# Kernel tuning notes

Hardware: AMD Instinct MI355X
Metric: run time of the kernel (lower is better)

## Reference

```python
import jax, jax.numpy as jnp
import numpy as np

NUM_HEADS = 8


def setup_inputs() -> dict:
    key = jax.random.key(0)
    B, T, N, C = 16, 24, 716, 256
    H = NUM_HEADS
    D = C // H
    ks = jax.random.split(key, 14)

    def w(k, shape, scale=0.02):
        return jax.random.normal(k, shape, dtype=jnp.float32) * scale

    return {
        "x": jax.random.normal(ks[0], (B, T, N, C), dtype=jnp.float32),
        # nn.Linear weights stored PyTorch-style [out, in]
        "Wq": w(ks[1], (C, C)), "bq": w(ks[2], (C,)),
        "Wk": w(ks[3], (C, C)), "bk": w(ks[4], (C,)),
        "Wv": w(ks[5], (C, C)), "bv": w(ks[6], (C,)),
        "Wo": w(ks[7], (C, C)), "bo": w(ks[8], (C,)),
        # grouped conv1d (kernel_size=1) weights, squeezed: [out_ch, in_ch_per_group]
        "w1": w(ks[9], (C, D)), "b1": w(ks[10], (C,)),
        "w2": w(ks[11], (3 * C, D)), "b2": w(ks[12], (3 * C,)),
    }


def reference(x, Wq, bq, Wk, bk, Wv, bv, Wo, bo, w1, b1, w2, b2):
    B, T, N, C = x.shape
    H = NUM_HEADS
    D = C // H
    BT = B * T
    scale = D ** -0.5

    xf = x.reshape(BT, N, C)
    # q, k, v: [BT, H, N, D]
    q = (xf @ Wq.T + bq).reshape(BT, N, H, D).transpose(0, 2, 1, 3)
    k = (xf @ Wk.T + bk).reshape(BT, N, H, D).transpose(0, 2, 1, 3)
    v = (xf @ Wv.T + bv).reshape(BT, N, H, D).transpose(0, 2, 1, 3)

    # linear attention: kv outer-product [BT, H, D, D], scaled by (scale/N)
    kv = jnp.einsum('bhnd,bhne->bhde', k, v) * (scale / N)
    attn = jnp.einsum('bhnd,bhde->bhne', q, kv)
    # mean-pooled correction term
    kmean = k.mean(axis=2)  # [BT, H, D]
    vmean = v.mean(axis=2)  # [BT, H, D]
    qk = jnp.einsum('bhnd,bhd->bhn', q, kmean) * scale  # [BT, H, N]
    xa = attn + (1.0 - qk)[..., None] * vmean[:, :, None, :]
    xa = xa.transpose(0, 2, 1, 3).reshape(BT, N, C)

    # dynamic per-channel 3-tap kernel weights from node-mean features
    m = xf.mean(axis=1).reshape(BT, H, D)  # grouped input [BT, H, D]
    h1 = jnp.einsum('bgi,goi->bgo', m, w1.reshape(H, D, D)) + b1.reshape(H, D)
    h1 = jax.nn.gelu(h1, approximate=False)
    h2 = jnp.einsum('bgi,goi->bgo', h1, w2.reshape(H, 3 * D, D)) + b2.reshape(H, 3 * D)
    rw = h2.reshape(BT, C, 3)  # per-(sample, channel) 3-tap kernel

    # depthwise conv1d over node axis with groups = BT*C (cross-correlation)
    vc = v.transpose(0, 1, 3, 2).reshape(BT, C, N)
    vp = jnp.pad(vc, ((0, 0), (0, 0), (1, 1)))
    res = (rw[:, :, 0:1] * vp[:, :, 0:N]
           + rw[:, :, 1:2] * vp[:, :, 1:N + 1]
           + rw[:, :, 2:3] * vp[:, :, 2:N + 2])  # [BT, C, N]

    out = (xa + res.transpose(0, 2, 1)).reshape(B, T, N, C)
    return out @ Wo.T + bo
```

## Files before the change

### kernel.cpp

```cpp
#include <hip/hip_runtime.h>
#include <hip/hip_bf16.h>
#include <math.h>

typedef __attribute__((ext_vector_type(8))) short short8;
typedef __attribute__((ext_vector_type(4))) short sv4;
typedef __attribute__((ext_vector_type(4))) float f32x4;
typedef unsigned int u32;

#define BT_ 384
#define N_ 716
#define C_ 256
#define H_ 8
#define D_ 32
#define MROWS (BT_ * N_)
#define NT_ (MROWS / 64)
#define SCALE_ 0.17677669529663687f
#define INVN_ (1.0f / 716.0f)

__device__ __forceinline__ void gload_lds16(const void* g, void* l) {
    __builtin_amdgcn_global_load_lds(
        (const __attribute__((address_space(1))) u32*)g,
        (__attribute__((address_space(3))) u32*)l, 16, 0, 0);
}

__global__ void prep_weights(const float* __restrict__ Wq, const float* __restrict__ bq,
                             const float* __restrict__ Wk, const float* __restrict__ bk,
                             const float* __restrict__ Wv, const float* __restrict__ bv,
                             const float* __restrict__ Wo,
                             __hip_bfloat16* __restrict__ wqkv, float* __restrict__ bqkv,
                             __hip_bfloat16* __restrict__ wo) {
    int idx = blockIdx.x * 256 + threadIdx.x;
    if (idx < 768 * 256) {
        int o = idx >> 8, c = idx & 255;
        const float* W = (o < 256) ? Wq : ((o < 512) ? Wk : Wv);
        int oo = o & 255;
        wqkv[idx] = __float2bfloat16(W[oo * 256 + c]);
    }
    if (idx < 256 * 256) wo[idx] = __float2bfloat16(Wo[idx]);
    if (idx < 768) bqkv[idx] = (idx < 256) ? bq[idx] : ((idx < 512) ? bk[idx - 256] : bv[idx - 512]);
}

__global__ __launch_bounds__(256)
void convert_x(const float* __restrict__ x, __hip_bfloat16* __restrict__ xb,
               float* __restrict__ msum) {
    int bt = blockIdx.x, chunk = blockIdx.y;
    int t = threadIdx.x;
    int c4 = (t & 63) * 4;
    int r0 = t >> 6;
    size_t base = ((size_t)bt * N_ + (size_t)chunk * 179) * C_;
    float s0 = 0.f, s1 = 0.f, s2 = 0.f, s3 = 0.f;
    for (int r = r0; r < 179; r += 4) {
        float4 f = *(const float4*)&x[base + (size_t)r * C_ + c4];
        union { sv4 v; __hip_bfloat16 h[4]; } u;
        u.h[0] = __float2bfloat16(f.x);
        u.h[1] = __float2bfloat16(f.y);
        u.h[2] = __float2bfloat16(f.z);
        u.h[3] = __float2bfloat16(f.w);
        *(sv4*)&xb[base + (size_t)r * C_ + c4] = u.v;
        s0 += f.x; s1 += f.y; s2 += f.z; s3 += f.w;
    }
    atomicAdd(&msum[bt * C_ + c4 + 0], s0);
    atomicAdd(&msum[bt * C_ + c4 + 1], s1);
    atomicAdd(&msum[bt * C_ + c4 + 2], s2);
    atomicAdd(&msum[bt * C_ + c4 + 3], s3);
}

__global__ __launch_bounds__(256)
void mlp_rw(const float* __restrict__ msum, const float* __restrict__ w1,
            const float* __restrict__ b1, const float* __restrict__ w2,
            const float* __restrict__ b2, float* __restrict__ rw) {
    int bt = blockIdx.x;
    int t = threadIdx.x;
    __shared__ float m_l[256];
    __shared__ float h1_l[256];
    m_l[t] = msum[bt * 256 + t] * INVN_;
    __syncthreads();
    int g = t >> 5;
    float a = b1[t];
    #pragma unroll
    for (int i = 0; i < 32; ++i) a += m_l[g * 32 + i] * w1[t * 32 + i];
    h1_l[t] = 0.5f * a * (1.0f + erff(a * 0.70710678118654752f));
    __syncthreads();
    for (int o = t; o < 768; o += 256) {
        int gg = o / 96;
        float s = b2[o];
        #pragma unroll
        for (int i = 0; i < 32; ++i) s += h1_l[gg * 32 + i] * w2[o * 32 + i];
        rw[bt * 768 + o] = s;
    }
}

template<int NCOLS, int GRIDX, bool OUT_BF16>
__global__ __launch_bounds__(256, 2)
void gemm_persist(const __hip_bfloat16* __restrict__ A, const __hip_bfloat16* __restrict__ Bm,
                  const float* __restrict__ bias, void* __restrict__ outp) {
    __shared__ __align__(16) __hip_bfloat16 As[2][64 * 256];
    const int L = blockIdx.x;
    const int xcd = L & 7, w = L >> 3;
    const int cb = w % GRIDX;
    const int ib = xcd * 32 + w / GRIDX;
    const int tid = threadIdx.x;
    const int lane = tid & 63;
    const int wave = tid >> 6;
    const int wn = wave;
    const int colBase = cb * 128;
    const int l15 = lane & 15, lq = lane >> 4;
    const int lrow2 = lane >> 5;
    const int p = lane & 31;

    auto stageA = [&](int rt, int buf) {
        #pragma unroll
        for (int i = 0; i < 8; ++i) {
            int r = wave * 16 + 2 * i + lrow2;
            const __hip_bfloat16* g = A + ((size_t)rt * 64 + r) * 256 + ((p ^ (r & 7)) * 8);
            gload_lds16(g, &As[buf][(wave * 16 + 2 * i) * 256]);
        }
    };

    stageA(ib, 0);

    short8 bf[2][8];
    #pragma unroll
    for (int n = 0; n < 2; ++n)
        #pragma unroll
        for (int ks = 0; ks < 8; ++ks)
            bf[n][ks] = *(const short8*)&Bm[(size_t)(colBase + wn * 32 + n * 16 + l15) * 256 + ks * 32 + lq * 8];
    float biasr[2];
    #pragma unroll
    for (int n = 0; n < 2; ++n)
        biasr[n] = bias[colBase + wn * 32 + n * 16 + l15];

    asm volatile("s_waitcnt vmcnt(0)" ::: "memory");
    __builtin_amdgcn_s_barrier();

    int buf = 0;
    for (int rt = ib; rt < NT_; rt += 256) {
        int rtn = rt + 256;
        if (rtn < NT_) stageA(rtn, buf ^ 1);

        f32x4 acc[4][2] = {};
        #pragma unroll
        for (int ks = 0; ks < 8; ++ks) {
            short8 af[4];
            #pragma unroll
            for (int m = 0; m < 4; ++m) {
                int row = m * 16 + l15;
                af[m] = *(const short8*)&As[buf][row * 256 + (((ks * 4 + lq) ^ (row & 7)) * 8)];
            }
            #pragma unroll
            for (int m = 0; m < 4; ++m)
                #pragma unroll
                for (int n = 0; n < 2; ++n)
                    acc[m][n] = __builtin_amdgcn_mfma_f32_16x16x32_bf16(af[m], bf[n][ks], acc[m][n], 0, 0, 0);
        }
        asm volatile("s_waitcnt lgkmcnt(0)" ::: "memory");
        __builtin_amdgcn_s_barrier();

        if constexpr (OUT_BF16) {
            __hip_bfloat16* Cs = &As[buf][0];
            #pragma unroll
            for (int m = 0; m < 4; ++m)
                #pragma unroll
                for (int n = 0; n < 2; ++n) {
                    int col = wn * 32 + n * 16 + l15;
                    #pragma unroll
                    for (int j = 0; j < 4; ++j)
                        Cs[(m * 16 + lq * 4 + j) * 136 + col] =
                            __float2bfloat16(acc[m][n][j] + biasr[n]);
                }
            asm volatile("s_waitcnt lgkmcnt(0)" ::: "memory");
            __builtin_amdgcn_s_barrier();
            int row = tid >> 2, cq = tid & 3;
            __hip_bfloat16* og = (__hip_bfloat16*)outp + ((size_t)rt * 64 + row) * NCOLS + colBase;
            #pragma unroll
            for (int i = 0; i < 4; ++i) {
                int col = cq * 8 + i * 32;
                *(short8*)&og[col] = *(const short8*)&Cs[row * 136 + col];
            }
            asm volatile("s_waitcnt vmcnt(2) lgkmcnt(0)" ::: "memory");
            __builtin_amdgcn_s_barrier();
        } else {
            float* Cs = (float*)&As[buf][0];
            #pragma unroll
            for (int pp = 0; pp < 2; ++pp) {
                #pragma unroll
                for (int mm = 0; mm < 2; ++mm) {
                    int m = 2 * pp + mm;
                    #pragma unroll
                    for (int n = 0; n < 2; ++n) {
                        int col = wn * 32 + n * 16 + l15;
                        #pragma unroll
                        for (int j = 0; j < 4; ++j)
                            Cs[(mm * 16 + lq * 4 + j) * 132 + col] = acc[m][n][j] + biasr[n];
                    }
                }
                asm volatile("s_waitcnt lgkmcnt(0)" ::: "memory");
                __builtin_amdgcn_s_barrier();
                int row = tid >> 3, k = tid & 7;
                float* og = (float*)outp + ((size_t)rt * 64 + pp * 32 + row) * NCOLS + colBase;
                #pragma unroll
                for (int i = 0; i < 4; ++i) {
                    int col = k * 4 + i * 32;
                    *(float4*)&og[col] = *(const float4*)&Cs[row * 132 + col];
                }
                asm volatile("s_waitcnt lgkmcnt(0)" ::: "memory");
                __builtin_amdgcn_s_barrier();
            }
            asm volatile("s_waitcnt vmcnt(4) lgkmcnt(0)" ::: "memory");
            __builtin_amdgcn_s_barrier();
        }
        buf ^= 1;
    }
}

__global__ __launch_bounds__(512, 2)
void reduce_kv(const __hip_bfloat16* __restrict__ qkv, __hip_bfloat16* __restrict__ kv2t,
               float* __restrict__ vmeanb) {
    __shared__ __align__(16) __hip_bfloat16 T[512 * 64];
    const int bt = blockIdx.x;
    const int tid = threadIdx.x;
    const int lane = tid & 63;
    const int h = tid >> 6;
    const int l15 = lane & 15, lq = lane >> 4;
    const int co = tid >> 3;
    const int np3 = tid & 7;
    const size_t rowbase = (size_t)bt * N_;

    union S8 { short8 v; unsigned short u[8]; };
    const short8 zero8 = {0, 0, 0, 0, 0, 0, 0, 0};

    auto issue_loads = [&](int n0, S8* Aq, S8* Bq) {
        #pragma unroll
        for (int s = 0; s < 4; ++s) {
            int n = n0 + 2 * (np3 + 8 * s);
            Aq[s].v = (n < N_)     ? *(const short8*)&qkv[(rowbase + n) * 768 + 256 + co * 8] : zero8;
            Bq[s].v = (n + 1 < N_) ? *(const short8*)&qkv[(rowbase + n + 1) * 768 + 256 + co * 8] : zero8;
        }
    };
    auto write_lds = [&](S8* Aq, S8* Bq) {
        #pragma unroll
        for (int s = 0; s < 4; ++s) {
            int r = 2 * (np3 + 8 * s);
            int slotbase = ((r >> 3));
            #pragma unroll
            for (int j = 0; j < 8; ++j) {
                int c = co * 8 + j;
                u32 wv = (u32)Aq[s].u[j] | ((u32)Bq[s].u[j] << 16);
                int off = c * 64 + ((slotbase ^ (c & 7)) << 3) + (r & 7);
                *(u32*)&T[off] = wv;
            }
        }
    };

    S8 bufA[4], bufB[4], nxtA[4], nxtB[4];
    issue_loads(0, bufA, bufB);

    f32x4 acc[2][2] = {};
    f32x4 acck[2] = {};
    f32x4 accv[2] = {};
    S8 ones;
    #pragma unroll
    for (int j = 0; j < 8; ++j) ones.u[j] = 0x3F80;

    for (int chunk = 0; chunk < 12; ++chunk) {
        if (chunk < 11) issue_loads((chunk + 1) * 64, nxtA, nxtB);
        write_lds(bufA, bufB);
        __syncthreads();
        #pragma unroll
        for (int nc = 0; nc < 2; ++nc) {
            short8 af[2], bfr[2];
            int slot = nc * 4 + lq;
            #pragma unroll
            for (int dh = 0; dh < 2; ++dh) {
                int c = h * 32 + dh * 16 + l15;
                af[dh] = *(const short8*)&T[c * 64 + ((slot ^ (c & 7)) << 3)];
            }
            #pragma unroll
            for (int eh = 0; eh < 2; ++eh) {
                int c = 256 + h * 32 + eh * 16 + l15;
                bfr[eh] = *(const short8*)&T[c * 64 + ((slot ^ (c & 7)) << 3)];
            }
            #pragma unroll
            for (int dh = 0; dh < 2; ++dh)
                #pragma unroll
                for (int eh = 0; eh < 2; ++eh)
                    acc[dh][eh] = __builtin_amdgcn_mfma_f32_16x16x32_bf16(af[dh], bfr[eh], acc[dh][eh], 0, 0, 0);
            #pragma unroll
            for (int dh = 0; dh < 2; ++dh)
                acck[dh] = __builtin_amdgcn_mfma_f32_16x16x32_bf16(af[dh], ones.v, acck[dh], 0, 0, 0);
            #pragma unroll
            for (int eh = 0; eh < 2; ++eh)
                accv[eh] = __builtin_amdgcn_mfma_f32_16x16x32_bf16(ones.v, bfr[eh], accv[eh], 0, 0, 0);
        }
        __syncthreads();
        #pragma unroll
        for (int s = 0; s < 4; ++s) { bufA[s] = nxtA[s]; bufB[s] = nxtB[s]; }
    }

    const int bh = bt * 8 + h;
    #pragma unroll
    for (int eh = 0; eh < 2; ++eh) {
        int e = eh * 16 + l15;
        float vme = accv[eh][0] * INVN_;
        #pragma unroll
        for (int dh = 0; dh < 2; ++dh) {
            union { sv4 v; __hip_bfloat16 x[4]; } o;
            #pragma unroll
            for (int j = 0; j < 4; ++j) {
                float km = acck[dh][j] * INVN_;
                float val = acc[dh][eh][j] * (SCALE_ * INVN_) - SCALE_ * km * vme;
                o.x[j] = __float2bfloat16(val);
            }
            *(sv4*)&kv2t[(size_t)bh * 1024 + e * 32 + dh * 16 + lq * 4] = o.v;
        }
        if (lq == 0) vmeanb[bh * 32 + e] = vme;
    }
}

__global__ __launch_bounds__(256)
void fuse_z2(const __hip_bfloat16* __restrict__ qkv, const __hip_bfloat16* __restrict__ kv2t,
             const float* __restrict__ vmeanb, const float* __restrict__ rw,
             __hip_bfloat16* __restrict__ Z) {
    __shared__ __align__(16) __hip_bfloat16 attn[64][256];
    __shared__ __align__(16) __hip_bfloat16 kvl[8192];
    int bt = blockIdx.x;
    int n0 = blockIdx.y * 64;
    int rows = (N_ - n0 < 64) ? (N_ - n0) : 64;
    int t = threadIdx.x;
    const size_t rowbase = (size_t)bt * N_;

    {
        const __hip_bfloat16* src = kv2t + (size_t)bt * 8192;
        #pragma unroll
        for (int i = 0; i < 4; ++i) {
            int off = (t + i * 256) * 8;
            *(short8*)&kvl[off] = *(const short8*)&src[off];
        }
    }
    __syncthreads();

    {
        int lane = t & 63, wave = t >> 6;
        int l15 = lane & 15, lq = lane >> 4;
        int r0 = wave * 16;
        int gn = n0 + r0 + l15; if (gn > N_ - 1) gn = N_ - 1;
        const __hip_bfloat16* qrow = qkv + (rowbase + gn) * 768;
        #pragma unroll
        for (int h = 0; h < 8; ++h) {
            short8 af = *(const short8*)&qrow[h * 32 + lq * 8];
            #pragma unroll
            for (int half = 0; half < 2; ++half) {
                short8 bfr = *(const short8*)&kvl[h * 1024 + (half * 16 + l15) * 32 + lq * 8];
                f32x4 acc = {};
                acc = __builtin_amdgcn_mfma_f32_16x16x32_bf16(af, bfr, acc, 0, 0, 0);
                int col = h * 32 + half * 16 + l15;
                float vm = vmeanb[bt * 256 + col];
                #pragma unroll
                for (int j = 0; j < 4; ++j)
                    attn[r0 + lq * 4 + j][col] = __float2bfloat16(acc[j] + vm);
            }
        }
    }
    __syncthreads();

    {
        int tr = t >> 5;
        int c8 = (t & 31) * 8;
        float w0[8], w1_[8], w2_[8];
        #pragma unroll
        for (int u = 0; u < 8; ++u) {
            w0[u]  = rw[bt * 768 + (c8 + u) * 3 + 0];
            w1_[u] = rw[bt * 768 + (c8 + u) * 3 + 1];
            w2_[u] = rw[bt * 768 + (c8 + u) * 3 + 2];
        }
        int rbeg = tr * 8;
        if (rbeg < rows) {
            int rend = rbeg + 8; if (rend > rows) rend = rows;
            union U8 { short8 v; __hip_bfloat16 h[8]; };
            auto loadv = [&](int gn, float* dst) {
                if (gn >= 0 && gn < N_) {
                    U8 u; u.v = *(const short8*)&qkv[(rowbase + gn) * 768 + 512 + c8];
                    #pragma unroll
                    for (int uu = 0; uu < 8; ++uu) dst[uu] = __bfloat162float(u.h[uu]);
                } else {
                    #pragma unroll
                    for (int uu = 0; uu < 8; ++uu) dst[uu] = 0.0f;
                }
            };
            float vprev[8], vcur[8], vnext[8];
            loadv(n0 + rbeg - 1, vprev);
            loadv(n0 + rbeg, vcur);
            for (int r = rbeg; r < rend; ++r) {
                int gn = n0 + r;
                loadv(gn + 1, vnext);
                U8 at; at.v = *(const short8*)&attn[r][c8];
                U8 zv;
                #pragma unroll
                for (int u = 0; u < 8; ++u) {
                    float s = __bfloat162float(at.h[u]) + w0[u] * vprev[u]
                              + w1_[u] * vcur[u] + w2_[u] * vnext[u];
                    zv.h[u] = __float2bfloat16(s);
                }
                *(short8*)&Z[(rowbase + gn) * 256 + c8] = zv.v;
                #pragma unroll
                for (int u = 0; u < 8; ++u) { vprev[u] = vcur[u]; vcur[u] = vnext[u]; }
            }
        }
    }
}

extern "C" void kernel_launch(void* const* d_in, const int* in_sizes, int n_in,
                              void* d_out, int out_size, void* d_ws, size_t ws_size,
                              hipStream_t stream) {
    (void)in_sizes; (void)n_in; (void)out_size; (void)ws_size;
    const float* x  = (const float*)d_in[0];
    const float* Wq = (const float*)d_in[1];  const float* bq = (const float*)d_in[2];
    const float* Wk = (const float*)d_in[3];  const float* bk = (const float*)d_in[4];
    const float* Wv = (const float*)d_in[5];  const float* bv = (const float*)d_in[6];
    const float* Wo = (const float*)d_in[7];  const float* bo = (const float*)d_in[8];
    const float* w1 = (const float*)d_in[9];  const float* b1 = (const float*)d_in[10];
    const float* w2 = (const float*)d_in[11]; const float* b2 = (const float*)d_in[12];
    float* out = (float*)d_out;

    char* ws = (char*)d_ws;
    size_t off = 0;
    auto take = [&](size_t bytes) -> char* {
        char* p = ws + off;
        off = (off + bytes + 255) & ~(size_t)255;
        return p;
    };

    __hip_bfloat16* qkv   = (__hip_bfloat16*)take((size_t)MROWS * 768 * 2);
    __hip_bfloat16* xb    = (__hip_bfloat16*)take((size_t)MROWS * 256 * 2);
    __hip_bfloat16* Zbuf  = xb;
    __hip_bfloat16* wqkv  = (__hip_bfloat16*)take(768 * 256 * 2);
    __hip_bfloat16* wo    = (__hip_bfloat16*)take(256 * 256 * 2);
    float* bqkv   = (float*)take(768 * 4);
    float* msum   = (float*)take(384 * 256 * 4);
    float* rw     = (float*)take(384 * 768 * 4);
    __hip_bfloat16* kv2t = (__hip_bfloat16*)take((size_t)384 * 8192 * 2);
    float* vmeanb = (float*)take(384 * 256 * 4);

    hipMemsetAsync(msum, 0, 384 * 256 * 4, stream);

    prep_weights<<<768, 256, 0, stream>>>(Wq, bq, Wk, bk, Wv, bv, Wo, wqkv, bqkv, wo);
    convert_x<<<dim3(384, 4), 256, 0, stream>>>(x, xb, msum);
    mlp_rw<<<384, 256, 0, stream>>>(msum, w1, b1, w2, b2, rw);
    gemm_persist<768, 6, true><<<1536, 256, 0, stream>>>(xb, wqkv, bqkv, qkv);
    reduce_kv<<<384, 512, 0, stream>>>(qkv, kv2t, vmeanb);
    fuse_z2<<<dim3(384, 12), 256, 0, stream>>>(qkv, kv2t, vmeanb, rw, Zbuf);
    gemm_persist<256, 2, false><<<512, 256, 0, stream>>>(Zbuf, wo, bo, out);
}
```

Measured before the change: 542.5 us.

## Fuse output projection GEMM into attention/conv epilogue kernel

Merges the Z-building kernel with the final Wo projection. Each 512-thread block keeps its 64x256 Z tile in swizzled LDS, holds Wo fragments in registers, runs the MFMA GEMM in place and writes fp32 output through an LDS staging buffer. This removes the bf16 Z round trip to global memory and one kernel launch. In exchange, every block reloads the full Wo matrix into registers, register pressure rises, and the 716-row tail tiles waste some MFMA work.

```diff
diff --git a/kernel.cpp b/kernel.cpp
--- a/kernel.cpp
+++ b/kernel.cpp
@@ -317,93 +317,155 @@
     }
 }
 
-__global__ __launch_bounds__(256)
-void fuse_z2(const __hip_bfloat16* __restrict__ qkv, const __hip_bfloat16* __restrict__ kv2t,
-             const float* __restrict__ vmeanb, const float* __restrict__ rw,
-             __hip_bfloat16* __restrict__ Z) {
-    __shared__ __align__(16) __hip_bfloat16 attn[64][256];
-    __shared__ __align__(16) __hip_bfloat16 kvl[8192];
-    int bt = blockIdx.x;
-    int n0 = blockIdx.y * 64;
-    int rows = (N_ - n0 < 64) ? (N_ - n0) : 64;
-    int t = threadIdx.x;
+__global__ __launch_bounds__(512, 2)
+void fuse_zout(const __hip_bfloat16* __restrict__ qkv, const __hip_bfloat16* __restrict__ kv2t,
+               const float* __restrict__ vmeanb, const float* __restrict__ rw,
+               const __hip_bfloat16* __restrict__ wo, const float* __restrict__ bo,
+               float* __restrict__ outp) {
+    __shared__ __align__(16) __hip_bfloat16 AZ[64 * 256];
+    __shared__ __align__(16) char RB[17408];
+    __hip_bfloat16* kvl = (__hip_bfloat16*)RB;
+
+    const int bt = blockIdx.x;
+    const int n0 = blockIdx.y * 64;
+    const int rows = (N_ - n0 < 64) ? (N_ - n0) : 64;
+    const int t = threadIdx.x;
+    const int lane = t & 63;
+    const int w = t >> 6;
+    const int l15 = lane & 15, lq = lane >> 4;
     const size_t rowbase = (size_t)bt * N_;
+
+    short8 bf[2][8];
+    #pragma unroll
+    for (int n = 0; n < 2; ++n)
+        #pragma unroll
+        for (int ks = 0; ks < 8; ++ks)
+            bf[n][ks] = *(const short8*)&wo[(size_t)(w * 32 + n * 16 + l15) * 256 + ks * 32 + lq * 8];
+    float biasr[2];
+    #pragma unroll
+    for (int n = 0; n < 2; ++n) biasr[n] = bo[w * 32 + n * 16 + l15];
 
     {
         const __hip_bfloat16* src = kv2t + (size_t)bt * 8192;
         #pragma unroll
-        for (int i = 0; i < 4; ++i) {
-            int off = (t + i * 256) * 8;
+        for (int i = 0; i < 2; ++i) {
+            int off = (t + i * 512) * 8;
             *(short8*)&kvl[off] = *(const short8*)&src[off];
         }
     }
     __syncthreads();
 
     {
-        int lane = t & 63, wave = t >> 6;
-        int l15 = lane & 15, lq = lane >> 4;
-        int r0 = wave * 16;
+        int r0 = (w & 3) * 16;
+        int hb = (w >> 2) * 4;
         int gn = n0 + r0 + l15; if (gn > N_ - 1) gn = N_ - 1;
         const __hip_bfloat16* qrow = qkv + (rowbase + gn) * 768;
         #pragma unroll
-        for (int h = 0; h < 8; ++h) {
+        for (int hh = 0; hh < 4; ++hh) {
+            int h = hb + hh;
             short8 af = *(const short8*)&qrow[h * 32 + lq * 8];
             #pragma unroll
             for (int half = 0; half < 2; ++half) {
-                short8 bfr = *(const short8*)&kvl[h * 1024 + (half * 16 + l15) * 32 + lq * 8];
-                f32x4 acc = {};
-                acc = __builtin_amdgcn_mfma_f32_16x16x32_bf16(af, bfr, acc, 0, 0, 0);
+                short8 kb = *(const short8*)&kvl[h * 1024 + (half * 16 + l15) * 32 + lq * 8];
+                f32x4 a = {};
+                a = __builtin_amdgcn_mfma_f32_16x16x32_bf16(af, kb, a, 0, 0, 0);
                 int col = h * 32 + half * 16 + l15;
                 float vm = vmeanb[bt * 256 + col];
                 #pragma unroll
-                for (int j = 0; j < 4; ++j)
-                    attn[r0 + lq * 4 + j][col] = __float2bfloat16(acc[j] + vm);
+                for (int j = 0; j < 4; ++j) {
+                    int r = r0 + lq * 4 + j;
+                    AZ[r * 256 + ((((col >> 3) ^ (r & 7)) << 3) | (col & 7))] =
+                        __float2bfloat16(a[j] + vm);
+                }
             }
         }
     }
     __syncthreads();
 
     {
-        int tr = t >> 5;
-        int c8 = (t & 31) * 8;
-        float w0[8], w1_[8], w2_[8];
-        #pragma unroll
-        for (int u = 0; u < 8; ++u) {
-            w0[u]  = rw[bt * 768 + (c8 + u) * 3 + 0];
-            w1_[u] = rw[bt * 768 + (c8 + u) * 3 + 1];
-            w2_[u] = rw[bt * 768 + (c8 + u) * 3 + 2];
-        }
-        int rbeg = tr * 8;
+        int rbeg = (t >> 6) * 8;
+        int c4 = (t & 63) * 4;
         if (rbeg < rows) {
             int rend = rbeg + 8; if (rend > rows) rend = rows;
-            union U8 { short8 v; __hip_bfloat16 h[8]; };
+            float w0[4], w1_[4], w2_[4];
+            #pragma unroll
+            for (int u = 0; u < 4; ++u) {
+                w0[u]  = rw[bt * 768 + (c4 + u) * 3 + 0];
+                w1_[u] = rw[bt * 768 + (c4 + u) * 3 + 1];
+                w2_[u] = rw[bt * 768 + (c4 + u) * 3 + 2];
+            }
+            union U4 { sv4 v; __hip_bfloat16 h[4]; };
             auto loadv = [&](int gn, float* dst) {
                 if (gn >= 0 && gn < N_) {
-                    U8 u; u.v = *(const short8*)&qkv[(rowbase + gn) * 768 + 512 + c8];
+                    U4 u; u.v = *(const sv4*)&qkv[(rowbase + gn) * 768 + 512 + c4];
                     #pragma unroll
-                    for (int uu = 0; uu < 8; ++uu) dst[uu] = __bfloat162float(u.h[uu]);
+                    for (int uu = 0; uu < 4; ++uu) dst[uu] = __bfloat162float(u.h[uu]);
                 } else {
                     #pragma unroll
-                    for (int uu = 0; uu < 8; ++uu) dst[uu] = 0.0f;
+                    for (int uu = 0; uu < 4; ++uu) dst[uu] = 0.0f;
                 }
             };
-            float vprev[8], vcur[8], vnext[8];
-            loadv(n0 + rbeg - 1, vprev);
-            loadv(n0 + rbeg, vcur);
+            float vp[4], vc[4], vn[4];
+            loadv(n0 + rbeg - 1, vp);
+            loadv(n0 + rbeg, vc);
             for (int r = rbeg; r < rend; ++r) {
                 int gn = n0 + r;
-                loadv(gn + 1, vnext);
-                U8 at; at.v = *(const short8*)&attn[r][c8];
-                U8 zv;
-                #pragma unroll
-                for (int u = 0; u < 8; ++u) {
-                    float s = __bfloat162float(at.h[u]) + w0[u] * vprev[u]
-                              + w1_[u] * vcur[u] + w2_[u] * vnext[u];
+                loadv(gn + 1, vn);
+                int base = r * 256 + ((((c4 >> 3) ^ (r & 7)) << 3) | (c4 & 7));
+                U4 az; az.v = *(const sv4*)&AZ[base];
+                U4 zv;
+                #pragma unroll
+                for (int u = 0; u < 4; ++u) {
+                    float s = __bfloat162float(az.h[u]) + w0[u] * vp[u]
+                              + w1_[u] * vc[u] + w2_[u] * vn[u];
                     zv.h[u] = __float2bfloat16(s);
                 }
-                *(short8*)&Z[(rowbase + gn) * 256 + c8] = zv.v;
-                #pragma unroll
-                for (int u = 0; u < 8; ++u) { vprev[u] = vcur[u]; vcur[u] = vnext[u]; }
+                *(sv4*)&AZ[base] = zv.v;
+                #pragma unroll
+                for (int u = 0; u < 4; ++u) { vp[u] = vc[u]; vc[u] = vn[u]; }
+            }
+        }
+    }
+    __syncthreads();
+
+    f32x4 acc[4][2] = {};
+    #pragma unroll
+    for (int ks = 0; ks < 8; ++ks) {
+        short8 af[4];
+        #pragma unroll
+        for (int m = 0; m < 4; ++m) {
+            int row = m * 16 + l15;
+            af[m] = *(const short8*)&AZ[row * 256 + (((ks * 4 + lq) ^ (row & 7)) << 3)];
+        }
+        #pragma unroll
+        for (int m = 0; m < 4; ++m)
+            #pragma unroll
+            for (int n = 0; n < 2; ++n)
+                acc[m][n] = __builtin_amdgcn_mfma_f32_16x16x32_bf16(af[m], bf[n][ks], acc[m][n], 0, 0, 0);
+    }
+
+    float* Cs = (float*)RB;
+    #pragma unroll
+    for (int pp = 0; pp < 4; ++pp) {
+        asm volatile("s_waitcnt lgkmcnt(0)" ::: "memory");
+        __builtin_amdgcn_s_barrier();
+        #pragma unroll
+        for (int n = 0; n < 2; ++n) {
+            int col = w * 32 + n * 16 + l15;
+            #pragma unroll
+            for (int j = 0; j < 4; ++j)
+                Cs[(lq * 4 + j) * 264 + col] = acc[pp][n][j] + biasr[n];
+        }
+        asm volatile("s_waitcnt lgkmcnt(0)" ::: "memory");
+        __builtin_amdgcn_s_barrier();
+        int row = t >> 5, kk = t & 31;
+        int grow = pp * 16 + row;
+        if (grow < rows) {
+            float* og = outp + (rowbase + n0 + grow) * 256;
+            #pragma unroll
+            for (int i = 0; i < 2; ++i) {
+                int col = kk * 4 + i * 128;
+                *(float4*)&og[col] = *(const float4*)&Cs[row * 264 + col];
             }
         }
     }
@@ -432,7 +494,6 @@
 
     __hip_bfloat16* qkv   = (__hip_bfloat16*)take((size_t)MROWS * 768 * 2);
     __hip_bfloat16* xb    = (__hip_bfloat16*)take((size_t)MROWS * 256 * 2);
-    __hip_bfloat16* Zbuf  = xb;
     __hip_bfloat16* wqkv  = (__hip_bfloat16*)take(768 * 256 * 2);
     __hip_bfloat16* wo    = (__hip_bfloat16*)take(256 * 256 * 2);
     float* bqkv   = (float*)take(768 * 4);
@@ -448,6 +509,5 @@
     mlp_rw<<<384, 256, 0, stream>>>(msum, w1, b1, w2, b2, rw);
     gemm_persist<768, 6, true><<<1536, 256, 0, stream>>>(xb, wqkv, bqkv, qkv);
     reduce_kv<<<384, 512, 0, stream>>>(qkv, kv2t, vmeanb);
-    fuse_z2<<<dim3(384, 12), 256, 0, stream>>>(qkv, kv2t, vmeanb, rw, Zbuf);
-    gemm_persist<256, 2, false><<<512, 256, 0, stream>>>(Zbuf, wo, bo, out);
-}
+    fuse_zout<<<dim3(384, 12), 512, 0, stream>>>(qkv, kv2t, vmeanb, rw, wo, bo, out);
+}
```

Measured after the change: 554.4 us. 1.02x slower.
